# Kernel tuning notes

Measured on AMD Instinct MI355X. Metric: run time of the kernel, lower is better.

The kernel has to match this reference:

```python
import jax, jax.numpy as jnp
import numpy as np

B, S, H, NH = 8, 2048, 128, 4
HS = H // NH
EPS = 1e-8


def setup_inputs() -> dict:
    key = jax.random.key(0)
    ks = jax.random.split(key, 20)
    sc = 1.0 / np.sqrt(H)
    d = {
        'item_embeds': jax.random.normal(ks[0], (B, S, H), jnp.float32),
        'behavior_embeds': jax.random.normal(ks[1], (B, S, H), jnp.float32),
        'attn_mask': jnp.zeros((B, 1, S, S), jnp.float32),
    }
    names = ['Wq', 'Wk', 'Wv', 'Wqb', 'Wkb', 'Wvb', 'Wf']
    for i, n in enumerate(names):
        d[n] = jax.random.normal(ks[2 + i], (H, H), jnp.float32) * sc
        d['b' + n[1:]] = jnp.zeros((H,), jnp.float32)
    d['ln_w'] = jnp.ones((H,), jnp.float32)
    d['ln_b'] = jnp.zeros((H,), jnp.float32)
    return d


def _split_heads(x):
    # [B,S,H] -> [B,NH,S,HS]
    return x.reshape(B, S, NH, HS).transpose(0, 2, 1, 3)


def _layer_norm(x, w, b):
    u = jnp.mean(x, -1, keepdims=True)
    s = jnp.mean((x - u) ** 2, -1, keepdims=True)
    return w * ((x - u) / jnp.sqrt(s + EPS)) + b


def reference(item_embeds, behavior_embeds, attn_mask,
              Wq, bq, Wk, bk, Wv, bv,
              Wqb, bqb, Wkb, bkb, Wvb, bvb,
              Wf, bf, ln_w, ln_b):
    Q = _split_heads(item_embeds @ Wq + bq)
    K = _split_heads(item_embeds @ Wk + bk)
    V = _split_heads(item_embeds @ Wv + bv)
    Qb = _split_heads(behavior_embeds @ Wqb + bqb)
    Kb = _split_heads(behavior_embeds @ Wkb + bkb)
    # V_behavior computed in the original forward but unused downstream
    _Vb = _split_heads(behavior_embeds @ Wvb + bvb)
    scores = (jnp.einsum('bhqd,bhkd->bhqk', Q, K)
              + jnp.einsum('bhqd,bhkd->bhqk', Qb, Kb)) / np.sqrt(HS)
    scores = scores + attn_mask
    probs = jax.nn.softmax(scores, axis=-1)
    attn_out = jnp.einsum('bhqk,bhkd->bhqd', probs, V)
    attn_out = attn_out.transpose(0, 2, 1, 3).reshape(B, S, H)
    out = attn_out @ Wf + bf
    return _layer_norm(out + item_embeds, ln_w, ln_b)
```

## Files before the change

### kernel.cpp

```cpp
#include <hip/hip_runtime.h>
#include <math.h>

typedef unsigned short ushort_t;
typedef __attribute__((ext_vector_type(8))) short bf16x8;
typedef __attribute__((ext_vector_type(4))) float f32x4;

namespace {
constexpr int B = 8, S = 2048, H = 128, NH = 4, HS = 32;
constexpr float EPS = 1e-8f;
constexpr float SCALE = 0.17677669529663687f;
constexpr int QT = 16, KT = 64;
constexpr int NE = B * S * H;
constexpr int NML = B * NH * S;
}

__device__ __forceinline__ ushort_t f2bf(float f) {
  unsigned u = __float_as_uint(f);
  unsigned r = (u + 0x7FFFu + ((u >> 16) & 1u)) >> 16;
  return (ushort_t)r;
}

__device__ __forceinline__ float bf2f(ushort_t u) {
  return __uint_as_float((unsigned)u << 16);
}

__device__ __forceinline__ f32x4 mfma16(bf16x8 a, bf16x8 b, f32x4 c) {
  return __builtin_amdgcn_mfma_f32_16x16x32_bf16(a, b, c, 0, 0, 0);
}

__global__ __launch_bounds__(256) void wcvt_kernel(
    const float* __restrict__ Wq, const float* __restrict__ Wk, const float* __restrict__ Wv,
    const float* __restrict__ Wqb, const float* __restrict__ Wkb, const float* __restrict__ Wf,
    ushort_t* __restrict__ Wt)
{
  const float* Ws[6] = {Wq, Wk, Wv, Wqb, Wkb, Wf};
  const float scl[6] = {SCALE, 1.f, 1.f, SCALE, 1.f, 1.f};
  const int m = blockIdx.y;
  const int kb = blockIdx.x;
  const float* W = Ws[m];
  const float sc = scl[m];
  __shared__ float T[32 * 132];
  const int t = threadIdx.x;
#pragma unroll
  for (int u = 0; u < 4; ++u) {
    const int idx = u * 256 + t;
    const int row = idx >> 5, c4 = idx & 31;
    const float4 v = *(const float4*)&W[(kb * 32 + row) * H + c4 * 4];
    *(float4*)&T[row * 132 + c4 * 4] = v;
  }
  __syncthreads();
#pragma unroll
  for (int u = 0; u < 16; ++u) {
    const int idx = u * 256 + t;
    const int n = idx >> 5, kk = idx & 31;
    Wt[m * (H * H) + n * H + kb * 32 + kk] = f2bf(T[kk * 132 + n] * sc);
  }
}

__global__ __launch_bounds__(256) void proj_kernel(
    const float* __restrict__ item, const float* __restrict__ beh,
    const ushort_t* __restrict__ Wt,
    const float* __restrict__ bq, const float* __restrict__ bk, const float* __restrict__ bv,
    const float* __restrict__ bqb, const float* __restrict__ bkb,
    ushort_t* __restrict__ Qo, ushort_t* __restrict__ Ko, ushort_t* __restrict__ Qbo,
    ushort_t* __restrict__ Kbo, ushort_t* __restrict__ Vto)
{
  __shared__ ushort_t Xs[32 * 136];
  __shared__ ushort_t Yb[32 * 136];
  const int t = threadIdx.x;
  const int p = blockIdx.y;
  const long r0 = (long)blockIdx.x * 32;
  const float* X = (p < 3) ? item : beh;
#pragma unroll
  for (int u = 0; u < 4; ++u) {
    const int idx = u * 256 + t;
    const int row = idx >> 5, c4 = idx & 31;
    const float4 v = *(const float4*)&X[(r0 + row) * H + c4 * 4];
    unsigned long long pk = (unsigned long long)f2bf(v.x) | ((unsigned long long)f2bf(v.y) << 16)
        | ((unsigned long long)f2bf(v.z) << 32) | ((unsigned long long)f2bf(v.w) << 48);
    *(unsigned long long*)&Xs[row * 136 + c4 * 4] = pk;
  }
  __syncthreads();

  const int w = t >> 6, l = t & 63, l15 = l & 15, quad = l >> 4;
  const int bb = (int)(r0 >> 11);
  const int s0 = (int)(r0 & (S - 1));
  const float* bias[5] = {bq, bk, bv, bqb, bkb};
  const float bscale[5] = {SCALE, 1.f, 1.f, SCALE, 1.f};
  ushort_t* dsts[5] = {Qo, Ko, Vto, Qbo, Kbo};

  bf16x8 af[2][4];
#pragma unroll
  for (int mt = 0; mt < 2; ++mt)
#pragma unroll
    for (int ks = 0; ks < 4; ++ks)
      af[mt][ks] = *(const bf16x8*)&Xs[(mt * 16 + l15) * 136 + ks * 32 + quad * 8];

  f32x4 acc[2][2];
#pragma unroll
  for (int nt = 0; nt < 2; ++nt) {
    const float bcol = bias[p][w * 32 + nt * 16 + l15] * bscale[p];
#pragma unroll
    for (int mt = 0; mt < 2; ++mt)
      acc[mt][nt] = (f32x4){bcol, bcol, bcol, bcol};
  }
  const ushort_t* Wp = Wt + p * (H * H);
#pragma unroll
  for (int ks = 0; ks < 4; ++ks) {
    bf16x8 bfr[2];
#pragma unroll
    for (int nt = 0; nt < 2; ++nt)
      bfr[nt] = *(const bf16x8*)&Wp[(w * 32 + nt * 16 + l15) * H + ks * 32 + quad * 8];
#pragma unroll
    for (int mt = 0; mt < 2; ++mt)
#pragma unroll
      for (int nt = 0; nt < 2; ++nt)
        acc[mt][nt] = mfma16(af[mt][ks], bfr[nt], acc[mt][nt]);
  }
#pragma unroll
  for (int mt = 0; mt < 2; ++mt)
#pragma unroll
    for (int nt = 0; nt < 2; ++nt)
#pragma unroll
      for (int r = 0; r < 4; ++r)
        Yb[(mt * 16 + quad * 4 + r) * 136 + w * 32 + nt * 16 + l15] = f2bf(acc[mt][nt][r]);
  __syncthreads();
  ushort_t* dst = dsts[p];
  if (p == 2) {
    const int d = t >> 1, sh = (t & 1) * 16;
    ushort_t tmp[16];
#pragma unroll
    for (int i = 0; i < 16; ++i) tmp[i] = Yb[(sh + i) * 136 + d];
    const long gidx = ((long)(bb * NH + (d >> 5)) * HS + (d & 31)) * S + s0 + sh;
    *(uint4*)&dst[gidx] = *(const uint4*)&tmp[0];
    *(uint4*)&dst[gidx + 8] = *(const uint4*)&tmp[8];
  } else {
    const int row = t >> 3, cb = (t & 7) * 16;
    const int h = cb >> 5, dd = cb & 31;
    const long gidx = ((long)(bb * NH + h) * S + s0 + row) * HS + dd;
    *(uint4*)&dst[gidx] = *(const uint4*)&Yb[row * 136 + cb];
    *(uint4*)&dst[gidx + 8] = *(const uint4*)&Yb[row * 136 + cb + 8];
  }
}

__global__ __launch_bounds__(256, 4) void attn_kernel(
    const ushort_t* __restrict__ Q, const ushort_t* __restrict__ K,
    const ushort_t* __restrict__ Qb, const ushort_t* __restrict__ Kb,
    const ushort_t* __restrict__ Vt, const float* __restrict__ mask,
    ushort_t* __restrict__ Op, float* __restrict__ Mp, float* __restrict__ Lp)
{
  __shared__ ushort_t Pb[NH][16 * 72];
  const int t = threadIdx.x;
  const int w = t >> 6;
  const int l = t & 63, l15 = l & 15, quad = l >> 4;
  const int q0 = blockIdx.x * QT;
  const int b = blockIdx.y;
  const int half_ = blockIdx.z;
  const long hQ = (long)(b * NH + w) * S * HS;
  const long hV = (long)(b * NH + w) * HS * S;

  const bf16x8 qf  = *(const bf16x8*)&Q[hQ + (long)(q0 + l15) * HS + quad * 8];
  const bf16x8 qbf = *(const bf16x8*)&Qb[hQ + (long)(q0 + l15) * HS + quad * 8];

  const float* mrow[4];
#pragma unroll
  for (int r = 0; r < 4; ++r)
    mrow[r] = mask + ((long)b * S + q0 + quad * 4 + r) * S + l15;

  float mold[4], lsum[4];
  f32x4 O[2];
#pragma unroll
  for (int r = 0; r < 4; ++r) { mold[r] = -1e30f; lsum[r] = 0.f; }
#pragma unroll
  for (int dt = 0; dt < 2; ++dt) O[dt] = (f32x4){0.f, 0.f, 0.f, 0.f};
  ushort_t* Pw = Pb[w];

  const int kt0 = half_ * (S / KT / 2), kt1 = kt0 + (S / KT / 2);
  for (int kt = kt0; kt < kt1; ++kt) {
    const int k0 = kt * KT;
    f32x4 sc[4];
#pragma unroll
    for (int nt = 0; nt < 4; ++nt)
#pragma unroll
      for (int r = 0; r < 4; ++r)
        sc[nt][r] = mrow[r][k0 + nt * 16];
    bf16x8 kf[4], kbf[4], vf[2][2];
#pragma unroll
    for (int nt = 0; nt < 4; ++nt) {
      kf[nt]  = *(const bf16x8*)&K[hQ + (long)(k0 + nt * 16 + l15) * HS + quad * 8];
      kbf[nt] = *(const bf16x8*)&Kb[hQ + (long)(k0 + nt * 16 + l15) * HS + quad * 8];
    }
#pragma unroll
    for (int dt = 0; dt < 2; ++dt)
#pragma unroll
      for (int ks = 0; ks < 2; ++ks)
        vf[dt][ks] = *(const bf16x8*)&Vt[hV + (long)(dt * 16 + l15) * S + k0 + ks * 32 + quad * 8];
#pragma unroll
    for (int nt = 0; nt < 4; ++nt) {
      sc[nt] = mfma16(qbf, kbf[nt], sc[nt]);
      sc[nt] = mfma16(qf, kf[nt], sc[nt]);
    }
    float alpha[4];
#pragma unroll
    for (int r = 0; r < 4; ++r) {
      float rm = fmaxf(fmaxf(sc[0][r], sc[1][r]), fmaxf(sc[2][r], sc[3][r]));
      rm = fmaxf(rm, __shfl_xor(rm, 1));
      rm = fmaxf(rm, __shfl_xor(rm, 2));
      rm = fmaxf(rm, __shfl_xor(rm, 4));
      rm = fmaxf(rm, __shfl_xor(rm, 8));
      const float mnew = fmaxf(mold[r], rm);
      alpha[r] = __expf(mold[r] - mnew);
      float rs = 0.f;
#pragma unroll
      for (int nt = 0; nt < 4; ++nt) {
        const float p = __expf(sc[nt][r] - mnew);
        sc[nt][r] = p;
        rs += p;
      }
      rs += __shfl_xor(rs, 1);
      rs += __shfl_xor(rs, 2);
      rs += __shfl_xor(rs, 4);
      rs += __shfl_xor(rs, 8);
      lsum[r] = lsum[r] * alpha[r] + rs;
      mold[r] = mnew;
    }
#pragma unroll
    for (int dt = 0; dt < 2; ++dt)
#pragma unroll
      for (int r = 0; r < 4; ++r)
        O[dt][r] *= alpha[r];
#pragma unroll
    for (int nt = 0; nt < 4; ++nt)
#pragma unroll
      for (int r = 0; r < 4; ++r)
        Pw[(quad * 4 + r) * 72 + nt * 16 + l15] = f2bf(sc[nt][r]);
    bf16x8 pf[2];
#pragma unroll
    for (int ks = 0; ks < 2; ++ks)
      pf[ks] = *(const bf16x8*)&Pw[l15 * 72 + ks * 32 + quad * 8];
#pragma unroll
    for (int dt = 0; dt < 2; ++dt)
#pragma unroll
      for (int ks = 0; ks < 2; ++ks)
        O[dt] = mfma16(pf[ks], vf[dt][ks], O[dt]);
  }
#pragma unroll
  for (int r = 0; r < 4; ++r) {
    const float inv = 1.f / lsum[r];
    const long row = (long)b * S + q0 + quad * 4 + r;
#pragma unroll
    for (int dt = 0; dt < 2; ++dt)
      Op[(long)half_ * NE + row * H + w * 32 + dt * 16 + l15] = f2bf(O[dt][r] * inv);
  }
  if (l15 == 0) {
#pragma unroll
    for (int r = 0; r < 4; ++r) {
      const long idx = ((long)(half_ * B + b) * NH + w) * S + q0 + quad * 4 + r;
      Mp[idx] = mold[r];
      Lp[idx] = lsum[r];
    }
  }
}

__global__ __launch_bounds__(256) void out_kernel(
    const ushort_t* __restrict__ Op, const float* __restrict__ Mp, const float* __restrict__ Lp,
    const float* __restrict__ item,
    const ushort_t* __restrict__ Wft, const float* __restrict__ bf_,
    const float* __restrict__ lnw, const float* __restrict__ lnb,
    float* __restrict__ out)
{
  __shared__ ushort_t As[16 * 136];
  __shared__ float Ys[16 * 132];
  const int t = threadIdx.x;
  const long r0 = (long)blockIdx.x * 16;
  {
    const int row = t >> 4, c8 = t & 15;
    const long g = r0 + row;
    const int bb = (int)(g >> 11);
    const int ss = (int)(g & (S - 1));
    const int col0 = c8 * 8;
    const int h = col0 >> 5;
    const long mlidx = ((long)bb * NH + h) * S + ss;
    const float m1 = Mp[mlidx], m2 = Mp[(long)NML + mlidx];
    const float l1 = Lp[mlidx], l2 = Lp[(long)NML + mlidx];
    const float M = fmaxf(m1, m2);
    const float w1 = l1 * __expf(m1 - M), w2 = l2 * __expf(m2 - M);
    const float inv = 1.f / (w1 + w2);
    const float wa = w1 * inv, wb = w2 * inv;
    const uint4 a1 = *(const uint4*)&Op[g * H + col0];
    const uint4 a2 = *(const uint4*)&Op[(long)NE + g * H + col0];
    const ushort_t* p1 = (const ushort_t*)&a1;
    const ushort_t* p2 = (const ushort_t*)&a2;
    ushort_t mg[8];
#pragma unroll
    for (int i = 0; i < 8; ++i)
      mg[i] = f2bf(bf2f(p1[i]) * wa + bf2f(p2[i]) * wb);
    *(uint4*)&As[row * 136 + col0] = *(const uint4*)&mg[0];
  }
  __syncthreads();
  const int w = t >> 6, l = t & 63, l15 = l & 15, quad = l >> 4;
  f32x4 acc[2];
#pragma unroll
  for (int nt = 0; nt < 2; ++nt) {
    const float bcol = bf_[w * 32 + nt * 16 + l15];
    acc[nt] = (f32x4){bcol, bcol, bcol, bcol};
  }
#pragma unroll
  for (int ks = 0; ks < 4; ++ks) {
    const bf16x8 a = *(const bf16x8*)&As[l15 * 136 + ks * 32 + quad * 8];
#pragma unroll
    for (int nt = 0; nt < 2; ++nt) {
      const bf16x8 bfr = *(const bf16x8*)&Wft[(w * 32 + nt * 16 + l15) * H + ks * 32 + quad * 8];
      acc[nt] = mfma16(a, bfr, acc[nt]);
    }
  }
#pragma unroll
  for (int nt = 0; nt < 2; ++nt)
#pragma unroll
    for (int r = 0; r < 4; ++r) {
      const int rl = quad * 4 + r;
      const int col = w * 32 + nt * 16 + l15;
      Ys[rl * 132 + col] = acc[nt][r] + item[(r0 + rl) * H + col];
    }
  __syncthreads();
  const int rl = t >> 4, ch = t & 15;
  float v[8];
#pragma unroll
  for (int g = 0; g < 2; ++g) {
    const float4 y = *(const float4*)&Ys[rl * 132 + ch * 8 + g * 4];
    v[g * 4 + 0] = y.x; v[g * 4 + 1] = y.y; v[g * 4 + 2] = y.z; v[g * 4 + 3] = y.w;
  }
  float s = 0.f;
#pragma unroll
  for (int i = 0; i < 8; ++i) s += v[i];
  s += __shfl_xor(s, 1);
  s += __shfl_xor(s, 2);
  s += __shfl_xor(s, 4);
  s += __shfl_xor(s, 8);
  const float u_ = s * (1.f / H);
  float s2 = 0.f;
#pragma unroll
  for (int i = 0; i < 8; ++i) { const float d = v[i] - u_; s2 += d * d; }
  s2 += __shfl_xor(s2, 1);
  s2 += __shfl_xor(s2, 2);
  s2 += __shfl_xor(s2, 4);
  s2 += __shfl_xor(s2, 8);
  const float rinv = rsqrtf(s2 * (1.f / H) + EPS);
#pragma unroll
  for (int g = 0; g < 2; ++g) {
    float4 o;
    const int col = ch * 8 + g * 4;
    o.x = lnw[col + 0] * ((v[g * 4 + 0] - u_) * rinv) + lnb[col + 0];
    o.y = lnw[col + 1] * ((v[g * 4 + 1] - u_) * rinv) + lnb[col + 1];
    o.z = lnw[col + 2] * ((v[g * 4 + 2] - u_) * rinv) + lnb[col + 2];
    o.w = lnw[col + 3] * ((v[g * 4 + 3] - u_) * rinv) + lnb[col + 3];
    *(float4*)&out[(r0 + rl) * H + col] = o;
  }
}

extern "C" void kernel_launch(void* const* d_in, const int* in_sizes, int n_in,
                              void* d_out, int out_size, void* d_ws, size_t ws_size,
                              hipStream_t stream) {
  const float* item = (const float*)d_in[0];
  const float* beh  = (const float*)d_in[1];
  const float* mask = (const float*)d_in[2];
  const float* Wq  = (const float*)d_in[3];  const float* bq  = (const float*)d_in[4];
  const float* Wk  = (const float*)d_in[5];  const float* bk  = (const float*)d_in[6];
  const float* Wv  = (const float*)d_in[7];  const float* bv  = (const float*)d_in[8];
  const float* Wqb = (const float*)d_in[9];  const float* bqb = (const float*)d_in[10];
  const float* Wkb = (const float*)d_in[11]; const float* bkb = (const float*)d_in[12];
  const float* Wf  = (const float*)d_in[15]; const float* bfv = (const float*)d_in[16];
  const float* lnw = (const float*)d_in[17]; const float* lnb = (const float*)d_in[18];
  float* out = (float*)d_out;

  ushort_t* ws = (ushort_t*)d_ws;
  ushort_t* Qw   = ws;
  ushort_t* Kw   = Qw + NE;
  ushort_t* Qbw  = Kw + NE;
  ushort_t* Kbw  = Qbw + NE;
  ushort_t* Vtw  = Kbw + NE;
  ushort_t* Opw  = Vtw + NE;
  ushort_t* Wt   = Opw + 2 * (long)NE;
  float* Mpw = (float*)(Wt + 6 * H * H);
  float* Lpw = Mpw + 2 * (long)NML;

  wcvt_kernel<<<dim3(4, 6), 256, 0, stream>>>(Wq, Wk, Wv, Wqb, Wkb, Wf, Wt);
  proj_kernel<<<dim3((B * S) / 32, 5), 256, 0, stream>>>(
      item, beh, Wt, bq, bk, bv, bqb, bkb, Qw, Kw, Qbw, Kbw, Vtw);
  attn_kernel<<<dim3(S / QT, B, 2), 256, 0, stream>>>(
      Qw, Kw, Qbw, Kbw, Vtw, mask, Opw, Mpw, Lpw);
  out_kernel<<<dim3((B * S) / 16), 256, 0, stream>>>(
      Opw, Mpw, Lpw, item, Wt + 5 * H * H, bfv, lnw, lnb, out);
}
```

Measured before the change: 401.7 us.

## Process two 16-row query chunks per wave to reuse K/V fragments

Each wave in the attention kernel now handles 32 query rows, as two 16-row chunks, instead of 16. The K, Kb and V fragments loaded per key tile are shared by both chunks, which halves global K/V traffic per query row and halves the grid. The cost is doubled register state (scores, O, softmax stats), so the occupancy target drops from 4 to 3 blocks and LDS use for P doubles. The mask read per element is unchanged and remains a large memory stream.

```diff
diff --git a/kernel.cpp b/kernel.cpp
--- a/kernel.cpp
+++ b/kernel.cpp
@@ -143,121 +143,148 @@
   }
 }
 
-__global__ __launch_bounds__(256, 4) void attn_kernel(
+__global__ __launch_bounds__(256, 3) void attn_kernel(
     const ushort_t* __restrict__ Q, const ushort_t* __restrict__ K,
     const ushort_t* __restrict__ Qb, const ushort_t* __restrict__ Kb,
     const ushort_t* __restrict__ Vt, const float* __restrict__ mask,
     ushort_t* __restrict__ Op, float* __restrict__ Mp, float* __restrict__ Lp)
 {
-  __shared__ ushort_t Pb[NH][16 * 72];
+  __shared__ ushort_t Pb[NH][2][16 * 72];
   const int t = threadIdx.x;
   const int w = t >> 6;
-  const int l = t & 63, l15 = l & 15, quad = l >> 4;
-  const int q0 = blockIdx.x * QT;
+  const int l = t & 63, l15 = l & 15, quad = l >> 4, quad4 = quad * 4;
+  const int q0 = blockIdx.x * 32;
   const int b = blockIdx.y;
   const int half_ = blockIdx.z;
   const long hQ = (long)(b * NH + w) * S * HS;
   const long hV = (long)(b * NH + w) * HS * S;
-
-  const bf16x8 qf  = *(const bf16x8*)&Q[hQ + (long)(q0 + l15) * HS + quad * 8];
-  const bf16x8 qbf = *(const bf16x8*)&Qb[hQ + (long)(q0 + l15) * HS + quad * 8];
-
-  const float* mrow[4];
-#pragma unroll
-  for (int r = 0; r < 4; ++r)
-    mrow[r] = mask + ((long)b * S + q0 + quad * 4 + r) * S + l15;
-
-  float mold[4], lsum[4];
-  f32x4 O[2];
-#pragma unroll
-  for (int r = 0; r < 4; ++r) { mold[r] = -1e30f; lsum[r] = 0.f; }
-#pragma unroll
-  for (int dt = 0; dt < 2; ++dt) O[dt] = (f32x4){0.f, 0.f, 0.f, 0.f};
-  ushort_t* Pw = Pb[w];
+  const ushort_t* Kp  = K + hQ;
+  const ushort_t* Kbp = Kb + hQ;
+  const ushort_t* Vp  = Vt + hV;
+
+  bf16x8 qf[2], qbf[2];
+#pragma unroll
+  for (int c = 0; c < 2; ++c) {
+    qf[c]  = *(const bf16x8*)&Q[hQ + (long)(q0 + c * 16 + l15) * HS + quad * 8];
+    qbf[c] = *(const bf16x8*)&Qb[hQ + (long)(q0 + c * 16 + l15) * HS + quad * 8];
+  }
+
+  const float* mrow[2][4];
+#pragma unroll
+  for (int c = 0; c < 2; ++c)
+#pragma unroll
+    for (int r = 0; r < 4; ++r)
+      mrow[c][r] = mask + ((long)b * S + q0 + c * 16 + quad4 + r) * S + l15;
+
+  float mold[2][4], lsum[2][4];
+  f32x4 O[2][2];
+#pragma unroll
+  for (int c = 0; c < 2; ++c) {
+#pragma unroll
+    for (int r = 0; r < 4; ++r) { mold[c][r] = -1e30f; lsum[c][r] = 0.f; }
+#pragma unroll
+    for (int dt = 0; dt < 2; ++dt) O[c][dt] = (f32x4){0.f, 0.f, 0.f, 0.f};
+  }
 
   const int kt0 = half_ * (S / KT / 2), kt1 = kt0 + (S / KT / 2);
   for (int kt = kt0; kt < kt1; ++kt) {
     const int k0 = kt * KT;
-    f32x4 sc[4];
-#pragma unroll
-    for (int nt = 0; nt < 4; ++nt)
-#pragma unroll
-      for (int r = 0; r < 4; ++r)
-        sc[nt][r] = mrow[r][k0 + nt * 16];
-    bf16x8 kf[4], kbf[4], vf[2][2];
+    bf16x8 kf[4], kbf[4];
 #pragma unroll
     for (int nt = 0; nt < 4; ++nt) {
-      kf[nt]  = *(const bf16x8*)&K[hQ + (long)(k0 + nt * 16 + l15) * HS + quad * 8];
-      kbf[nt] = *(const bf16x8*)&Kb[hQ + (long)(k0 + nt * 16 + l15) * HS + quad * 8];
-    }
+      kf[nt]  = *(const bf16x8*)&Kp[(long)(k0 + nt * 16 + l15) * HS + quad * 8];
+      kbf[nt] = *(const bf16x8*)&Kbp[(long)(k0 + nt * 16 + l15) * HS + quad * 8];
+    }
+    f32x4 sc[2][4];
+#pragma unroll
+    for (int c = 0; c < 2; ++c)
+#pragma unroll
+      for (int nt = 0; nt < 4; ++nt)
+#pragma unroll
+        for (int r = 0; r < 4; ++r)
+          sc[c][nt][r] = mrow[c][r][k0 + nt * 16];
+#pragma unroll
+    for (int c = 0; c < 2; ++c)
+#pragma unroll
+      for (int nt = 0; nt < 4; ++nt) {
+        sc[c][nt] = mfma16(qbf[c], kbf[nt], sc[c][nt]);
+        sc[c][nt] = mfma16(qf[c], kf[nt], sc[c][nt]);
+      }
+    bf16x8 vf[2][2];
 #pragma unroll
     for (int dt = 0; dt < 2; ++dt)
 #pragma unroll
       for (int ks = 0; ks < 2; ++ks)
-        vf[dt][ks] = *(const bf16x8*)&Vt[hV + (long)(dt * 16 + l15) * S + k0 + ks * 32 + quad * 8];
-#pragma unroll
-    for (int nt = 0; nt < 4; ++nt) {
-      sc[nt] = mfma16(qbf, kbf[nt], sc[nt]);
-      sc[nt] = mfma16(qf, kf[nt], sc[nt]);
-    }
-    float alpha[4];
+        vf[dt][ks] = *(const bf16x8*)&Vp[(long)(dt * 16 + l15) * S + k0 + ks * 32 + quad * 8];
+#pragma unroll
+    for (int c = 0; c < 2; ++c) {
+      float alpha[4];
+#pragma unroll
+      for (int r = 0; r < 4; ++r) {
+        float rm = fmaxf(fmaxf(sc[c][0][r], sc[c][1][r]), fmaxf(sc[c][2][r], sc[c][3][r]));
+        rm = fmaxf(rm, __shfl_xor(rm, 1));
+        rm = fmaxf(rm, __shfl_xor(rm, 2));
+        rm = fmaxf(rm, __shfl_xor(rm, 4));
+        rm = fmaxf(rm, __shfl_xor(rm, 8));
+        const float mnew = fmaxf(mold[c][r], rm);
+        alpha[r] = __expf(mold[c][r] - mnew);
+        float rs = 0.f;
+#pragma unroll
+        for (int nt = 0; nt < 4; ++nt) {
+          const float p = __expf(sc[c][nt][r] - mnew);
+          sc[c][nt][r] = p;
+          rs += p;
+        }
+        rs += __shfl_xor(rs, 1);
+        rs += __shfl_xor(rs, 2);
+        rs += __shfl_xor(rs, 4);
+        rs += __shfl_xor(rs, 8);
+        lsum[c][r] = lsum[c][r] * alpha[r] + rs;
+        mold[c][r] = mnew;
+      }
+#pragma unroll
+      for (int dt = 0; dt < 2; ++dt)
+#pragma unroll
+        for (int r = 0; r < 4; ++r)
+          O[c][dt][r] *= alpha[r];
+      ushort_t* Pw = Pb[w][c];
+#pragma unroll
+      for (int nt = 0; nt < 4; ++nt)
+#pragma unroll
+        for (int r = 0; r < 4; ++r)
+          Pw[(quad4 + r) * 72 + nt * 16 + l15] = f2bf(sc[c][nt][r]);
+    }
+#pragma unroll
+    for (int c = 0; c < 2; ++c) {
+      const ushort_t* Pw = Pb[w][c];
+      bf16x8 pf[2];
+#pragma unroll
+      for (int ks = 0; ks < 2; ++ks)
+        pf[ks] = *(const bf16x8*)&Pw[l15 * 72 + ks * 32 + quad * 8];
+#pragma unroll
+      for (int dt = 0; dt < 2; ++dt)
+#pragma unroll
+        for (int ks = 0; ks < 2; ++ks)
+          O[c][dt] = mfma16(pf[ks], vf[dt][ks], O[c][dt]);
+    }
+  }
+#pragma unroll
+  for (int c = 0; c < 2; ++c) {
 #pragma unroll
     for (int r = 0; r < 4; ++r) {
-      float rm = fmaxf(fmaxf(sc[0][r], sc[1][r]), fmaxf(sc[2][r], sc[3][r]));
-      rm = fmaxf(rm, __shfl_xor(rm, 1));
-      rm = fmaxf(rm, __shfl_xor(rm, 2));
-      rm = fmaxf(rm, __shfl_xor(rm, 4));
-      rm = fmaxf(rm, __shfl_xor(rm, 8));
-      const float mnew = fmaxf(mold[r], rm);
-      alpha[r] = __expf(mold[r] - mnew);
-      float rs = 0.f;
-#pragma unroll
-      for (int nt = 0; nt < 4; ++nt) {
-        const float p = __expf(sc[nt][r] - mnew);
-        sc[nt][r] = p;
-        rs += p;
+      const float inv = 1.f / lsum[c][r];
+      const long row = (long)b * S + q0 + c * 16 + quad4 + r;
+#pragma unroll
+      for (int dt = 0; dt < 2; ++dt)
+        Op[(long)half_ * NE + row * H + w * 32 + dt * 16 + l15] = f2bf(O[c][dt][r] * inv);
+    }
+    if (l15 == 0) {
+#pragma unroll
+      for (int r = 0; r < 4; ++r) {
+        const long idx = ((long)(half_ * B + b) * NH + w) * S + q0 + c * 16 + quad4 + r;
+        Mp[idx] = mold[c][r];
+        Lp[idx] = lsum[c][r];
       }
-      rs += __shfl_xor(rs, 1);
-      rs += __shfl_xor(rs, 2);
-      rs += __shfl_xor(rs, 4);
-      rs += __shfl_xor(rs, 8);
-      lsum[r] = lsum[r] * alpha[r] + rs;
-      mold[r] = mnew;
-    }
-#pragma unroll
-    for (int dt = 0; dt < 2; ++dt)
-#pragma unroll
-      for (int r = 0; r < 4; ++r)
-        O[dt][r] *= alpha[r];
-#pragma unroll
-    for (int nt = 0; nt < 4; ++nt)
-#pragma unroll
-      for (int r = 0; r < 4; ++r)
-        Pw[(quad * 4 + r) * 72 + nt * 16 + l15] = f2bf(sc[nt][r]);
-    bf16x8 pf[2];
-#pragma unroll
-    for (int ks = 0; ks < 2; ++ks)
-      pf[ks] = *(const bf16x8*)&Pw[l15 * 72 + ks * 32 + quad * 8];
-#pragma unroll
-    for (int dt = 0; dt < 2; ++dt)
-#pragma unroll
-      for (int ks = 0; ks < 2; ++ks)
-        O[dt] = mfma16(pf[ks], vf[dt][ks], O[dt]);
-  }
-#pragma unroll
-  for (int r = 0; r < 4; ++r) {
-    const float inv = 1.f / lsum[r];
-    const long row = (long)b * S + q0 + quad * 4 + r;
-#pragma unroll
-    for (int dt = 0; dt < 2; ++dt)
-      Op[(long)half_ * NE + row * H + w * 32 + dt * 16 + l15] = f2bf(O[dt][r] * inv);
-  }
-  if (l15 == 0) {
-#pragma unroll
-    for (int r = 0; r < 4; ++r) {
-      const long idx = ((long)(half_ * B + b) * NH + w) * S + q0 + quad * 4 + r;
-      Mp[idx] = mold[r];
-      Lp[idx] = lsum[r];
     }
   }
 }
@@ -387,7 +414,7 @@
   wcvt_kernel<<<dim3(4, 6), 256, 0, stream>>>(Wq, Wk, Wv, Wqb, Wkb, Wf, Wt);
   proj_kernel<<<dim3((B * S) / 32, 5), 256, 0, stream>>>(
       item, beh, Wt, bq, bk, bv, bqb, bkb, Qw, Kw, Qbw, Kbw, Vtw);
-  attn_kernel<<<dim3(S / QT, B, 2), 256, 0, stream>>>(
+  attn_kernel<<<dim3(S / 32, B, 2), 256, 0, stream>>>(
       Qw, Kw, Qbw, Kbw, Vtw, mask, Opw, Mpw, Lpw);
   out_kernel<<<dim3((B * S) / 16), 256, 0, stream>>>(
       Opw, Mpw, Lpw, item, Wt + 5 * H * H, bfv, lnw, lnb, out);
```

After: 362.4 us. -9.8%, faster.
